# Kernel tuning notes

Hardware: AMD Instinct MI355X
Metric: run time of the kernel (lower is better)

Reference implementation:

```python
import jax, jax.numpy as jnp
import numpy as np

N = 100000      # num nodes
E = 1600000     # num edges (avg degree 16)
IN = 128        # in_channels
OUT = 64        # out_channels
HID = 2 * OUT   # conv1 output width = 2*out_channels


def setup_inputs() -> dict:
    key = jax.random.key(0)
    k0, k1, k2, k3 = jax.random.split(key, 4)
    x = jax.random.uniform(k0, (N, IN), dtype=jnp.float32)
    edge_index = jax.random.randint(k1, (2, E), 0, N, dtype=jnp.int32)
    # GCNConv weights (glorot-style uniform), biases zero-init as in PyG
    s1 = float(np.sqrt(6.0 / (IN + HID)))
    W1 = jax.random.uniform(k2, (IN, HID), minval=-s1, maxval=s1, dtype=jnp.float32)
    b1 = jnp.zeros((HID,), dtype=jnp.float32)
    s2 = float(np.sqrt(6.0 / (HID + OUT)))
    W2 = jax.random.uniform(k3, (HID, OUT), minval=-s2, maxval=s2, dtype=jnp.float32)
    b2 = jnp.zeros((OUT,), dtype=jnp.float32)
    return {"x": x, "edge_index": edge_index, "W1": W1, "b1": b1, "W2": W2, "b2": b2}


def gcn_conv(x, W, b, src, dst, n):
    """PyG GCNConv: self-loops + symmetric deg^-1/2 normalization + scatter-add."""
    h = x @ W                                   # [n, d_out] dense transform first
    loops = jnp.arange(n, dtype=src.dtype)
    s = jnp.concatenate([src, loops])           # [E+n] sources (with self-loops)
    d = jnp.concatenate([dst, loops])           # [E+n] destinations
    deg = jax.ops.segment_sum(jnp.ones_like(s, dtype=h.dtype), d, num_segments=n)
    dinv = jnp.where(deg > 0, jax.lax.rsqrt(deg), 0.0)
    norm = dinv[s] * dinv[d]                    # [E+n]
    # gather -> scale -> scatter-add aggregation
    out = jax.ops.segment_sum(h[s] * norm[:, None], d, num_segments=n)
    return out + b


def reference(x, edge_index, W1, b1, W2, b2):
    src, dst = edge_index[0], edge_index[1]
    n = x.shape[0]
    h = jax.nn.relu(gcn_conv(x, W1, b1, src, dst, n))
    return gcn_conv(h, W2, b2, src, dst, n)
```

## Files before the change

kernel.cpp:

```cpp
#include <hip/hip_runtime.h>

#define IN_C  128
#define HID_C 128
#define OUT_C 64
#define NPB      128
#define NPB_SH   7
#define NPB_MASK 127
#define MAXB     2048
#define CAP      6144
#define B1_CHUNK 8192

typedef __attribute__((ext_vector_type(8))) short short8;
typedef __attribute__((ext_vector_type(4))) float f32x4;

__device__ __forceinline__ unsigned short f2bf(float f) {
    unsigned u = __float_as_uint(f);
    unsigned r = (u + 0x7FFFu + ((u >> 16) & 1u)) >> 16;
    return (unsigned short)r;
}
__device__ __forceinline__ float bf_lo(unsigned u) { return __uint_as_float(u << 16); }
__device__ __forceinline__ float bf_hi(unsigned u) { return __uint_as_float(u & 0xFFFF0000u); }


__global__ __launch_bounds__(256) void hist_kernel(const int* __restrict__ dst,
                                                   int* __restrict__ bhist,
                                                   int E, int B) {
    __shared__ int lh[MAXB];
    int t = threadIdx.x;
    int e0 = blockIdx.x * B1_CHUNK;
    int nE = min(B1_CHUNK, E - e0);
    if (B <= MAXB) {
        for (int i = t; i < B; i += 256) lh[i] = 0;
        __syncthreads();
        for (int i = t; i < nE; i += 256) atomicAdd(&lh[dst[e0 + i] >> NPB_SH], 1);
        __syncthreads();
        for (int i = t; i < B; i += 256)
            if (lh[i]) atomicAdd(&bhist[i], lh[i]);
    } else {
        for (int i = t; i < nE; i += 256) atomicAdd(&bhist[dst[e0 + i] >> NPB_SH], 1);
    }
}

__global__ __launch_bounds__(1024) void scan_bucket_kernel(const int* __restrict__ bhist,
                                                           int* __restrict__ bbase,
                                                           int* __restrict__ bcur, int B) {
    __shared__ int sums[1024];
    int t = threadIdx.x;
    int chunk = (B + 1023) >> 10;
    int beg = t * chunk, end = min(beg + chunk, B);
    int s = 0;
    for (int i = beg; i < end; ++i) s += bhist[i];
    sums[t] = s;
    __syncthreads();
    for (int off = 1; off < 1024; off <<= 1) {
        int v = (t >= off) ? sums[t - off] : 0;
        __syncthreads();
        sums[t] += v;
        __syncthreads();
    }
    int run = (t == 0) ? 0 : sums[t - 1];
    for (int i = beg; i < end; ++i) {
        bbase[i] = run; bcur[i] = run;
        run += bhist[i];
    }
    if (t == 1023) bbase[B] = sums[1023];
}

__global__ __launch_bounds__(256) void bucket_kernel(const int* __restrict__ src,
                                                     const int* __restrict__ dst,
                                                     int* __restrict__ bcur,
                                                     int* __restrict__ ebuf,
                                                     int E, int B) {
    __shared__ int hist[MAXB];
    __shared__ int runb[MAXB];
    int t = threadIdx.x;
    int e0 = blockIdx.x * B1_CHUNK;
    int nE = min(B1_CHUNK, E - e0);
    if (B <= MAXB) {
        for (int i = t; i < B; i += 256) hist[i] = 0;
        __syncthreads();
        for (int i = t; i < nE; i += 256) atomicAdd(&hist[dst[e0 + i] >> NPB_SH], 1);
        __syncthreads();
        for (int i = t; i < B; i += 256) {
            int c = hist[i];
            runb[i] = c ? atomicAdd(&bcur[i], c) : 0;
            hist[i] = 0;
        }
        __syncthreads();
        for (int i = t; i < nE; i += 256) {
            int d = dst[e0 + i], s = src[e0 + i];
            int b = d >> NPB_SH;
            int off2 = atomicAdd(&hist[b], 1);
            ebuf[runb[b] + off2] = (s << NPB_SH) | (d & NPB_MASK);
        }
    } else {
        for (int i = t; i < nE; i += 256) {
            int d = dst[e0 + i], s = src[e0 + i];
            int pos = atomicAdd(&bcur[d >> NPB_SH], 1);
            ebuf[pos] = (s << NPB_SH) | (d & NPB_MASK);
        }
    }
}

__global__ __launch_bounds__(256) void csr_kernel(const int* __restrict__ ebuf,
                                                  const int* __restrict__ bbase,
                                                  int* __restrict__ col,
                                                  int* __restrict__ rowptr,
                                                  float* __restrict__ dinv,
                                                  int N, int E) {
    __shared__ int sorted[CAP];
    __shared__ int lhist[NPB];
    __shared__ int lpre[NPB + 1];
    int b = blockIdx.x;
    int t = threadIdx.x;
    int base = bbase[b], size = bbase[b + 1] - base;
    int node_base = b << NPB_SH;
    int nn = min(NPB, N - node_base);

    if (t < NPB) lhist[t] = 0;
    __syncthreads();
    for (int i = t; i < size; i += 256) atomicAdd(&lhist[ebuf[base + i] & NPB_MASK], 1);
    __syncthreads();
    if (t < NPB) lpre[t + 1] = lhist[t];
    if (t == 0) lpre[0] = 0;
    __syncthreads();
    for (int off = 1; off < NPB; off <<= 1) {
        int v = (t >= off && t < NPB) ? lpre[t + 1 - off] : 0;
        __syncthreads();
        if (t < NPB) lpre[t + 1] += v;
        __syncthreads();
    }
    if (t < nn) {
        rowptr[node_base + t] = base + lpre[t];
        dinv[node_base + t] = rsqrtf((float)(lhist[t] + 1));
    }
    if (node_base + nn == N && t == 0) rowptr[N] = base + size;
    if (t < NPB) lhist[t] = lpre[t];
    __syncthreads();
    if (size <= CAP) {
        for (int i = t; i < size; i += 256) {
            int entry = ebuf[base + i];
            int slot = atomicAdd(&lhist[entry & NPB_MASK], 1);
            sorted[slot] = entry >> NPB_SH;
        }
        __syncthreads();
        for (int i = t; i < size; i += 256) col[base + i] = sorted[i];
    } else {
        for (int i = t; i < size; i += 256) {
            int entry = ebuf[base + i];
            int slot = atomicAdd(&lhist[entry & NPB_MASK], 1);
            col[base + slot] = entry >> NPB_SH;
        }
    }
}


template<int C, typename InT>
__global__ __launch_bounds__(256) void mm_mfma_kernel(
    const InT* __restrict__ X, const float* __restrict__ W,
    const float* __restrict__ dinv, unsigned short* __restrict__ Hs, int n) {
    constexpr int LD = 136;
    __shared__ unsigned short Wt[C][LD];
    int t = threadIdx.x;

    for (int i = t; i < (128 * C) / 4; i += 256) {
        int idx = i * 4;
        int k = idx / C, c = idx % C;
        float4 wv = *(const float4*)&W[(size_t)k * C + c];
        Wt[c + 0][k] = f2bf(wv.x);
        Wt[c + 1][k] = f2bf(wv.y);
        Wt[c + 2][k] = f2bf(wv.z);
        Wt[c + 3][k] = f2bf(wv.w);
    }
    __syncthreads();

    int w = t >> 6, lane = t & 63;
    int m = lane & 15, quad = lane >> 4;
    int row0 = blockIdx.x * 64 + w * 16;
    int arow = min(row0 + m, n - 1);

    constexpr int NT = C / 16;
    f32x4 acc[NT];
#pragma unroll
    for (int ct = 0; ct < NT; ++ct) acc[ct] = (f32x4){0.f, 0.f, 0.f, 0.f};

#pragma unroll
    for (int kk = 0; kk < 4; ++kk) {
        int k0 = kk * 32 + quad * 8;
        short8 a;
        if constexpr (sizeof(InT) == 4) {
            const float* xp = (const float*)X + (size_t)arow * 128 + k0;
            float4 f0 = *(const float4*)xp;
            float4 f1 = *(const float4*)(xp + 4);
            a[0] = (short)f2bf(f0.x); a[1] = (short)f2bf(f0.y);
            a[2] = (short)f2bf(f0.z); a[3] = (short)f2bf(f0.w);
            a[4] = (short)f2bf(f1.x); a[5] = (short)f2bf(f1.y);
            a[6] = (short)f2bf(f1.z); a[7] = (short)f2bf(f1.w);
        } else {
            a = *(const short8*)((const unsigned short*)X + (size_t)arow * 128 + k0);
        }
#pragma unroll
        for (int ct = 0; ct < NT; ++ct) {
            short8 b = *(const short8*)&Wt[ct * 16 + m][k0];
            acc[ct] = __builtin_amdgcn_mfma_f32_16x16x32_bf16(a, b, acc[ct], 0, 0, 0);
        }
    }

    int qrow = row0 + quad * 4;
    float dv[4];
#pragma unroll
    for (int r = 0; r < 4; ++r) dv[r] = (qrow + r < n) ? dinv[qrow + r] : 0.f;
#pragma unroll
    for (int ct = 0; ct < NT; ++ct) {
        int c = ct * 16 + m;
#pragma unroll
        for (int r = 0; r < 4; ++r) {
            int row = qrow + r;
            if (row < n) Hs[(size_t)row * C + c] = f2bf(acc[ct][r] * dv[r]);
        }
    }
}


template<int C, bool BOUT>
__global__ __launch_bounds__(256) void agg_kernel(
    const unsigned short* __restrict__ Hs, const float* __restrict__ bias,
    const float* __restrict__ dinv, const int* __restrict__ rowptr,
    const int* __restrict__ col, void* __restrict__ outv, int n, int relu) {
    constexpr int LPR = C / 8;
    constexpr int SLOTS = 64 / LPR;
    int d = (blockIdx.x * 256 + threadIdx.x) >> 6;
    if (d >= n) return;
    int lane = threadIdx.x & 63;
    int cl = lane & (LPR - 1);
    int slot = lane / LPR;

    float acc[8] = {0.f, 0.f, 0.f, 0.f, 0.f, 0.f, 0.f, 0.f};
    int beg = rowptr[d], end = rowptr[d + 1];

    for (int j0 = beg; j0 < end; j0 += 64) {
        int cnt = min(64, end - j0);
        int colv = (j0 + lane < end) ? col[j0 + lane] : 0;
        int groups = (cnt + SLOTS - 1) / SLOTS;
        for (int g = 0; g < groups; g += 4) {
            uint4 v[4];
#pragma unroll
            for (int b = 0; b < 4; ++b) {
                int e = (g + b) * SLOTS + slot;
                int idx = __shfl(colv, e & 63, 64);
                bool ok = (g + b < groups) && (e < cnt);
                v[b] = ok ? *((const uint4*)(Hs + (size_t)idx * C) + cl)
                          : make_uint4(0, 0, 0, 0);
            }
#pragma unroll
            for (int b = 0; b < 4; ++b) {
                acc[0] += bf_lo(v[b].x); acc[1] += bf_hi(v[b].x);
                acc[2] += bf_lo(v[b].y); acc[3] += bf_hi(v[b].y);
                acc[4] += bf_lo(v[b].z); acc[5] += bf_hi(v[b].z);
                acc[6] += bf_lo(v[b].w); acc[7] += bf_hi(v[b].w);
            }
        }
    }
#pragma unroll
    for (int mk = LPR; mk < 64; mk <<= 1) {
#pragma unroll
        for (int k = 0; k < 8; ++k) acc[k] += __shfl_xor(acc[k], mk, 64);
    }
    uint4 sv = *((const uint4*)(Hs + (size_t)d * C) + cl);
    acc[0] += bf_lo(sv.x); acc[1] += bf_hi(sv.x);
    acc[2] += bf_lo(sv.y); acc[3] += bf_hi(sv.y);
    acc[4] += bf_lo(sv.z); acc[5] += bf_hi(sv.z);
    acc[6] += bf_lo(sv.w); acc[7] += bf_hi(sv.w);

    float dv = dinv[d];
    float4 b0 = *((const float4*)bias + cl * 2);
    float4 b1 = *((const float4*)bias + cl * 2 + 1);
    float r[8];
    r[0] = dv * acc[0] + b0.x; r[1] = dv * acc[1] + b0.y;
    r[2] = dv * acc[2] + b0.z; r[3] = dv * acc[3] + b0.w;
    r[4] = dv * acc[4] + b1.x; r[5] = dv * acc[5] + b1.y;
    r[6] = dv * acc[6] + b1.z; r[7] = dv * acc[7] + b1.w;
    if (relu) {
#pragma unroll
        for (int k = 0; k < 8; ++k) r[k] = fmaxf(r[k], 0.f);
    }
    if (slot == 0) {
        if constexpr (BOUT) {
            uint4 o;
            o.x = (unsigned)f2bf(r[0]) | ((unsigned)f2bf(r[1]) << 16);
            o.y = (unsigned)f2bf(r[2]) | ((unsigned)f2bf(r[3]) << 16);
            o.z = (unsigned)f2bf(r[4]) | ((unsigned)f2bf(r[5]) << 16);
            o.w = (unsigned)f2bf(r[6]) | ((unsigned)f2bf(r[7]) << 16);
            *(uint4*)((unsigned short*)outv + (size_t)d * C + cl * 8) = o;
        } else {
            float* o = (float*)outv + (size_t)d * C + cl * 8;
            *(float4*)o = make_float4(r[0], r[1], r[2], r[3]);
            *(float4*)(o + 4) = make_float4(r[4], r[5], r[6], r[7]);
        }
    }
}


extern "C" void kernel_launch(void* const* d_in, const int* in_sizes, int n_in,
                              void* d_out, int out_size, void* d_ws, size_t ws_size,
                              hipStream_t stream) {
    const float* x  = (const float*)d_in[0];
    const int*   ei = (const int*)d_in[1];
    const float* W1 = (const float*)d_in[2];
    const float* b1 = (const float*)d_in[3];
    const float* W2 = (const float*)d_in[4];
    const float* b2 = (const float*)d_in[5];
    float* out = (float*)d_out;

    int N = in_sizes[0] / IN_C;
    int E = in_sizes[1] / 2;
    const int* src = ei;
    const int* dst = ei + E;
    int B = (N + NPB - 1) >> NPB_SH;

    char* ws = (char*)d_ws;
    size_t off = 0;
    int*   bhist  = (int*)(ws + off);   off += (size_t)B * 4;
    int*   bbase  = (int*)(ws + off);   off += (size_t)(B + 1) * 4;
    int*   bcur   = (int*)(ws + off);   off += (size_t)B * 4;
    float* dinv   = (float*)(ws + off); off += (size_t)N * 4;
    int*   rowptr = (int*)(ws + off);   off += (size_t)(N + 1) * 4;
    off = (off + 15) & ~(size_t)15;
    int*   ebuf   = (int*)(ws + off);   off += (size_t)E * 4;
    int*   col    = (int*)(ws + off);   off += (size_t)E * 4;
    off = (off + 15) & ~(size_t)15;
    unsigned short* H1  = (unsigned short*)(ws + off); off += (size_t)N * HID_C * 2;
    off = (off + 15) & ~(size_t)15;
    unsigned short* AG1 = (unsigned short*)(ws + off); off += (size_t)N * HID_C * 2;
    unsigned short* H2 = H1;

    hipMemsetAsync(bhist, 0, (size_t)B * 4, stream);

    int nblk = (E + B1_CHUNK - 1) / B1_CHUNK;
    hist_kernel<<<nblk, 256, 0, stream>>>(dst, bhist, E, B);
    scan_bucket_kernel<<<1, 1024, 0, stream>>>(bhist, bbase, bcur, B);
    bucket_kernel<<<nblk, 256, 0, stream>>>(src, dst, bcur, ebuf, E, B);
    csr_kernel<<<B, 256, 0, stream>>>(ebuf, bbase, col, rowptr, dinv, N, E);

    int mblk = (N + 63) / 64;
    mm_mfma_kernel<HID_C, float><<<mblk, 256, 0, stream>>>(x, W1, dinv, H1, N);
    agg_kernel<HID_C, true><<<(N + 3) / 4, 256, 0, stream>>>(H1, b1, dinv, rowptr, col, AG1, N, 1);

    mm_mfma_kernel<OUT_C, unsigned short><<<mblk, 256, 0, stream>>>(AG1, W2, dinv, H2, N);
    agg_kernel<OUT_C, false><<<(N + 3) / 4, 256, 0, stream>>>(H2, b2, dinv, rowptr, col, out, N, 0);
}
```

Measured before the change: 328.3 us.

## Store hidden features in 16-column slices and aggregate per slice

Intermediate bf16 feature matrices are stored as column slices of 16 features ([slice][node][16]), and the aggregation kernel is rewritten so each block handles one slice for 128 nodes, with two threads per node walking the neighbour list serially. The aim is to keep each slice's working set (about 3.2 MB for 100k nodes) resident in cache during the random gathers. The cost is that the neighbour list is re-read once per slice, and load balance across threads now follows per-node degree instead of a wave-cooperative layout. Nontemporal loads and stores are also used for the CSR and output streams.

New measurement: 419.8 us. +27.9%, slower.

```diff
diff --git a/kernel.cpp b/kernel.cpp
--- a/kernel.cpp
+++ b/kernel.cpp
@@ -12,6 +12,7 @@
 
 typedef __attribute__((ext_vector_type(8))) short short8;
 typedef __attribute__((ext_vector_type(4))) float f32x4;
+typedef __attribute__((ext_vector_type(4))) unsigned int u32x4;
 
 __device__ __forceinline__ unsigned short f2bf(float f) {
     unsigned u = __float_as_uint(f);
@@ -197,7 +198,9 @@
             a[4] = (short)f2bf(f1.x); a[5] = (short)f2bf(f1.y);
             a[6] = (short)f2bf(f1.z); a[7] = (short)f2bf(f1.w);
         } else {
-            a = *(const short8*)((const unsigned short*)X + (size_t)arow * 128 + k0);
+            const unsigned short* xp = (const unsigned short*)X;
+            int slice = k0 >> 4;
+            a = *(const short8*)(xp + (size_t)slice * n * 16 + (size_t)arow * 16 + (k0 & 15));
         }
 #pragma unroll
         for (int ct = 0; ct < NT; ++ct) {
@@ -212,69 +215,71 @@
     for (int r = 0; r < 4; ++r) dv[r] = (qrow + r < n) ? dinv[qrow + r] : 0.f;
 #pragma unroll
     for (int ct = 0; ct < NT; ++ct) {
-        int c = ct * 16 + m;
+        unsigned short* hp = Hs + (size_t)ct * n * 16 + m;
 #pragma unroll
         for (int r = 0; r < 4; ++r) {
             int row = qrow + r;
-            if (row < n) Hs[(size_t)row * C + c] = f2bf(acc[ct][r] * dv[r]);
+            if (row < n) hp[(size_t)row * 16] = f2bf(acc[ct][r] * dv[r]);
         }
     }
 }
 
 
 template<int C, bool BOUT>
-__global__ __launch_bounds__(256) void agg_kernel(
+__global__ __launch_bounds__(256) void agg_slice_kernel(
     const unsigned short* __restrict__ Hs, const float* __restrict__ bias,
     const float* __restrict__ dinv, const int* __restrict__ rowptr,
     const int* __restrict__ col, void* __restrict__ outv, int n, int relu) {
-    constexpr int LPR = C / 8;
-    constexpr int SLOTS = 64 / LPR;
-    int d = (blockIdx.x * 256 + threadIdx.x) >> 6;
+    constexpr int NS = C / 16;
+    int sb = blockIdx.x % NS;
+    int blk = blockIdx.x / NS;
+    int d = blk * 128 + (threadIdx.x >> 1);
     if (d >= n) return;
-    int lane = threadIdx.x & 63;
-    int cl = lane & (LPR - 1);
-    int slot = lane / LPR;
-
-    float acc[8] = {0.f, 0.f, 0.f, 0.f, 0.f, 0.f, 0.f, 0.f};
-    int beg = rowptr[d], end = rowptr[d + 1];
-
-    for (int j0 = beg; j0 < end; j0 += 64) {
-        int cnt = min(64, end - j0);
-        int colv = (j0 + lane < end) ? col[j0 + lane] : 0;
-        int groups = (cnt + SLOTS - 1) / SLOTS;
-        for (int g = 0; g < groups; g += 4) {
-            uint4 v[4];
-#pragma unroll
-            for (int b = 0; b < 4; ++b) {
-                int e = (g + b) * SLOTS + slot;
-                int idx = __shfl(colv, e & 63, 64);
-                bool ok = (g + b < groups) && (e < cnt);
-                v[b] = ok ? *((const uint4*)(Hs + (size_t)idx * C) + cl)
-                          : make_uint4(0, 0, 0, 0);
-            }
-#pragma unroll
-            for (int b = 0; b < 4; ++b) {
-                acc[0] += bf_lo(v[b].x); acc[1] += bf_hi(v[b].x);
-                acc[2] += bf_lo(v[b].y); acc[3] += bf_hi(v[b].y);
-                acc[4] += bf_lo(v[b].z); acc[5] += bf_hi(v[b].z);
-                acc[6] += bf_lo(v[b].w); acc[7] += bf_hi(v[b].w);
-            }
-        }
-    }
-#pragma unroll
-    for (int mk = LPR; mk < 64; mk <<= 1) {
-#pragma unroll
-        for (int k = 0; k < 8; ++k) acc[k] += __shfl_xor(acc[k], mk, 64);
-    }
-    uint4 sv = *((const uint4*)(Hs + (size_t)d * C) + cl);
-    acc[0] += bf_lo(sv.x); acc[1] += bf_hi(sv.x);
-    acc[2] += bf_lo(sv.y); acc[3] += bf_hi(sv.y);
-    acc[4] += bf_lo(sv.z); acc[5] += bf_hi(sv.z);
-    acc[6] += bf_lo(sv.w); acc[7] += bf_hi(sv.w);
+    int half = threadIdx.x & 1;
+    const unsigned short* hsl = Hs + (size_t)sb * n * 16;
+
+    int beg = __builtin_nontemporal_load(&rowptr[d]);
+    int end = __builtin_nontemporal_load(&rowptr[d + 1]);
+
+    float acc[8];
+    uint4 v0 = *((const uint4*)(hsl + (size_t)d * 16) + half);
+    acc[0] = bf_lo(v0.x); acc[1] = bf_hi(v0.x);
+    acc[2] = bf_lo(v0.y); acc[3] = bf_hi(v0.y);
+    acc[4] = bf_lo(v0.z); acc[5] = bf_hi(v0.z);
+    acc[6] = bf_lo(v0.w); acc[7] = bf_hi(v0.w);
+
+    int j = beg;
+    for (; j + 4 <= end; j += 4) {
+        int c0 = __builtin_nontemporal_load(col + j);
+        int c1 = __builtin_nontemporal_load(col + j + 1);
+        int c2 = __builtin_nontemporal_load(col + j + 2);
+        int c3 = __builtin_nontemporal_load(col + j + 3);
+        uint4 v[4];
+        v[0] = *((const uint4*)(hsl + (size_t)c0 * 16) + half);
+        v[1] = *((const uint4*)(hsl + (size_t)c1 * 16) + half);
+        v[2] = *((const uint4*)(hsl + (size_t)c2 * 16) + half);
+        v[3] = *((const uint4*)(hsl + (size_t)c3 * 16) + half);
+#pragma unroll
+        for (int b = 0; b < 4; ++b) {
+            acc[0] += bf_lo(v[b].x); acc[1] += bf_hi(v[b].x);
+            acc[2] += bf_lo(v[b].y); acc[3] += bf_hi(v[b].y);
+            acc[4] += bf_lo(v[b].z); acc[5] += bf_hi(v[b].z);
+            acc[6] += bf_lo(v[b].w); acc[7] += bf_hi(v[b].w);
+        }
+    }
+    for (; j < end; ++j) {
+        int c0 = __builtin_nontemporal_load(col + j);
+        uint4 v = *((const uint4*)(hsl + (size_t)c0 * 16) + half);
+        acc[0] += bf_lo(v.x); acc[1] += bf_hi(v.x);
+        acc[2] += bf_lo(v.y); acc[3] += bf_hi(v.y);
+        acc[4] += bf_lo(v.z); acc[5] += bf_hi(v.z);
+        acc[6] += bf_lo(v.w); acc[7] += bf_hi(v.w);
+    }
 
     float dv = dinv[d];
-    float4 b0 = *((const float4*)bias + cl * 2);
-    float4 b1 = *((const float4*)bias + cl * 2 + 1);
+    const float* bp = bias + sb * 16 + half * 8;
+    float4 b0 = *(const float4*)bp;
+    float4 b1 = *(const float4*)(bp + 4);
     float r[8];
     r[0] = dv * acc[0] + b0.x; r[1] = dv * acc[1] + b0.y;
     r[2] = dv * acc[2] + b0.z; r[3] = dv * acc[3] + b0.w;
@@ -284,19 +289,20 @@
 #pragma unroll
         for (int k = 0; k < 8; ++k) r[k] = fmaxf(r[k], 0.f);
     }
-    if (slot == 0) {
-        if constexpr (BOUT) {
-            uint4 o;
-            o.x = (unsigned)f2bf(r[0]) | ((unsigned)f2bf(r[1]) << 16);
-            o.y = (unsigned)f2bf(r[2]) | ((unsigned)f2bf(r[3]) << 16);
-            o.z = (unsigned)f2bf(r[4]) | ((unsigned)f2bf(r[5]) << 16);
-            o.w = (unsigned)f2bf(r[6]) | ((unsigned)f2bf(r[7]) << 16);
-            *(uint4*)((unsigned short*)outv + (size_t)d * C + cl * 8) = o;
-        } else {
-            float* o = (float*)outv + (size_t)d * C + cl * 8;
-            *(float4*)o = make_float4(r[0], r[1], r[2], r[3]);
-            *(float4*)(o + 4) = make_float4(r[4], r[5], r[6], r[7]);
-        }
+    if constexpr (BOUT) {
+        u32x4 o;
+        o.x = (unsigned)f2bf(r[0]) | ((unsigned)f2bf(r[1]) << 16);
+        o.y = (unsigned)f2bf(r[2]) | ((unsigned)f2bf(r[3]) << 16);
+        o.z = (unsigned)f2bf(r[4]) | ((unsigned)f2bf(r[5]) << 16);
+        o.w = (unsigned)f2bf(r[6]) | ((unsigned)f2bf(r[7]) << 16);
+        u32x4* op = (u32x4*)((unsigned short*)outv + (size_t)sb * n * 16 + (size_t)d * 16 + half * 8);
+        __builtin_nontemporal_store(o, op);
+    } else {
+        float* o = (float*)outv + (size_t)d * C + sb * 16 + half * 8;
+        f32x4 o0 = {r[0], r[1], r[2], r[3]};
+        f32x4 o1 = {r[4], r[5], r[6], r[7]};
+        __builtin_nontemporal_store(o0, (f32x4*)o);
+        __builtin_nontemporal_store(o1, (f32x4*)o + 1);
     }
 }
 
@@ -343,9 +349,13 @@
     csr_kernel<<<B, 256, 0, stream>>>(ebuf, bbase, col, rowptr, dinv, N, E);
 
     int mblk = (N + 63) / 64;
+    int ablk = (N + 127) >> 7;
+
     mm_mfma_kernel<HID_C, float><<<mblk, 256, 0, stream>>>(x, W1, dinv, H1, N);
-    agg_kernel<HID_C, true><<<(N + 3) / 4, 256, 0, stream>>>(H1, b1, dinv, rowptr, col, AG1, N, 1);
+    agg_slice_kernel<HID_C, true><<<ablk * (HID_C / 16), 256, 0, stream>>>(
+        H1, b1, dinv, rowptr, col, AG1, N, 1);
 
     mm_mfma_kernel<OUT_C, unsigned short><<<mblk, 256, 0, stream>>>(AG1, W2, dinv, H2, N);
-    agg_kernel<OUT_C, false><<<(N + 3) / 4, 256, 0, stream>>>(H2, b2, dinv, rowptr, col, out, N, 0);
-}
+    agg_slice_kernel<OUT_C, false><<<ablk * (OUT_C / 16), 256, 0, stream>>>(
+        H2, b2, dinv, rowptr, col, out, N, 0);
+}
```

## Pad CSR rows to multiples of 16 with zero-row sentinel to remove gather predication

Applied to the files above, without the earlier changes.

Each node's neighbour list is padded up to a multiple of 16 entries, and the padding points at an extra all-zero row appended to H. This lets the aggregation loop drop per-edge bounds checks and run full unrolled gather groups. The separate ebuf is removed so bucketing and CSR sorting work in place in col. The bucket chunk and shared-memory sort capacity are also retuned. The trade-off is extra padded gathers of the zero row and a larger col array. The in-place fallback path for oversized buckets only handles up to 32 entries per thread.

Result: slower. 347.3 us (+5.8%).

```diff
diff --git a/kernel.cpp b/kernel.cpp
--- a/kernel.cpp
+++ b/kernel.cpp
@@ -7,8 +7,10 @@
 #define NPB_SH   7
 #define NPB_MASK 127
 #define MAXB     2048
-#define CAP      6144
-#define B1_CHUNK 8192
+#define CAP      8192
+#define B1_CHUNK 4096
+#define PADQ     16
+#define PADSLACK ((PADQ - 1) * NPB)
 
 typedef __attribute__((ext_vector_type(8))) short short8;
 typedef __attribute__((ext_vector_type(4))) float f32x4;
@@ -60,7 +62,8 @@
     }
     int run = (t == 0) ? 0 : sums[t - 1];
     for (int i = beg; i < end; ++i) {
-        bbase[i] = run; bcur[i] = run;
+        bbase[i] = run;
+        bcur[i] = run + i * PADSLACK;
         run += bhist[i];
     }
     if (t == 1023) bbase[B] = sums[1023];
@@ -69,7 +72,7 @@
 __global__ __launch_bounds__(256) void bucket_kernel(const int* __restrict__ src,
                                                      const int* __restrict__ dst,
                                                      int* __restrict__ bcur,
-                                                     int* __restrict__ ebuf,
+                                                     int* __restrict__ col,
                                                      int E, int B) {
     __shared__ int hist[MAXB];
     __shared__ int runb[MAXB];
@@ -91,21 +94,21 @@
             int d = dst[e0 + i], s = src[e0 + i];
             int b = d >> NPB_SH;
             int off2 = atomicAdd(&hist[b], 1);
-            ebuf[runb[b] + off2] = (s << NPB_SH) | (d & NPB_MASK);
+            col[runb[b] + off2] = (s << NPB_SH) | (d & NPB_MASK);
         }
     } else {
         for (int i = t; i < nE; i += 256) {
             int d = dst[e0 + i], s = src[e0 + i];
             int pos = atomicAdd(&bcur[d >> NPB_SH], 1);
-            ebuf[pos] = (s << NPB_SH) | (d & NPB_MASK);
-        }
-    }
-}
-
-__global__ __launch_bounds__(256) void csr_kernel(const int* __restrict__ ebuf,
+            col[pos] = (s << NPB_SH) | (d & NPB_MASK);
+        }
+    }
+}
+
+__global__ __launch_bounds__(256) void csr_kernel(int* __restrict__ col,
                                                   const int* __restrict__ bbase,
-                                                  int* __restrict__ col,
                                                   int* __restrict__ rowptr,
+                                                  int* __restrict__ rowend,
                                                   float* __restrict__ dinv,
                                                   int N, int E) {
     __shared__ int sorted[CAP];
@@ -113,15 +116,16 @@
     __shared__ int lpre[NPB + 1];
     int b = blockIdx.x;
     int t = threadIdx.x;
-    int base = bbase[b], size = bbase[b + 1] - base;
+    int size = bbase[b + 1] - bbase[b];
+    int pbase = bbase[b] + b * PADSLACK;
     int node_base = b << NPB_SH;
     int nn = min(NPB, N - node_base);
 
     if (t < NPB) lhist[t] = 0;
     __syncthreads();
-    for (int i = t; i < size; i += 256) atomicAdd(&lhist[ebuf[base + i] & NPB_MASK], 1);
-    __syncthreads();
-    if (t < NPB) lpre[t + 1] = lhist[t];
+    for (int i = t; i < size; i += 256) atomicAdd(&lhist[col[pbase + i] & NPB_MASK], 1);
+    __syncthreads();
+    if (t < NPB) lpre[t + 1] = (lhist[t] + PADQ - 1) & ~(PADQ - 1);
     if (t == 0) lpre[0] = 0;
     __syncthreads();
     for (int off = 1; off < NPB; off <<= 1) {
@@ -131,25 +135,35 @@
         __syncthreads();
     }
     if (t < nn) {
-        rowptr[node_base + t] = base + lpre[t];
+        rowptr[node_base + t] = pbase + lpre[t];
+        rowend[node_base + t] = pbase + lpre[t + 1];
         dinv[node_base + t] = rsqrtf((float)(lhist[t] + 1));
     }
-    if (node_base + nn == N && t == 0) rowptr[N] = base + size;
     if (t < NPB) lhist[t] = lpre[t];
     __syncthreads();
-    if (size <= CAP) {
+    int psize = lpre[NPB];
+    if (psize <= CAP) {
+        for (int i = t; i < psize; i += 256) sorted[i] = N;
+        __syncthreads();
         for (int i = t; i < size; i += 256) {
-            int entry = ebuf[base + i];
+            int entry = col[pbase + i];
             int slot = atomicAdd(&lhist[entry & NPB_MASK], 1);
             sorted[slot] = entry >> NPB_SH;
         }
         __syncthreads();
-        for (int i = t; i < size; i += 256) col[base + i] = sorted[i];
+        for (int i = t; i < psize; i += 256) col[pbase + i] = sorted[i];
     } else {
-        for (int i = t; i < size; i += 256) {
-            int entry = ebuf[base + i];
+        int ent[32];
+        int c2 = 0;
+        for (int i = t; i < size && c2 < 32; i += 256) ent[c2++] = col[pbase + i];
+        __syncthreads();
+        for (int i = t; i < psize; i += 256) col[pbase + i] = N;
+        __syncthreads();
+        c2 = 0;
+        for (int i = t; i < size && c2 < 32; i += 256) {
+            int entry = ent[c2++];
             int slot = atomicAdd(&lhist[entry & NPB_MASK], 1);
-            col[base + slot] = entry >> NPB_SH;
+            col[pbase + slot] = entry >> NPB_SH;
         }
     }
 }
@@ -162,6 +176,11 @@
     constexpr int LD = 136;
     __shared__ unsigned short Wt[C][LD];
     int t = threadIdx.x;
+
+    if (blockIdx.x == 0) {
+        for (int i = t; i < C / 2; i += 256)
+            ((unsigned*)(Hs + (size_t)n * C))[i] = 0;
+    }
 
     for (int i = t; i < (128 * C) / 4; i += 256) {
         int idx = i * 4;
@@ -222,11 +241,28 @@
 }
 
 
+#define GBODY(NB)                                                              \
+    {                                                                          \
+        uint4 v[NB];                                                           \
+        _Pragma("unroll") for (int b = 0; b < NB; ++b) {                       \
+            int e = (g + b) * SLOTS + slot;                                    \
+            int idx = __shfl(colv, e, 64);                                     \
+            v[b] = *((const uint4*)(Hs + (size_t)idx * C) + cl);               \
+        }                                                                      \
+        _Pragma("unroll") for (int b = 0; b < NB; ++b) {                       \
+            acc[0] += bf_lo(v[b].x); acc[1] += bf_hi(v[b].x);                  \
+            acc[2] += bf_lo(v[b].y); acc[3] += bf_hi(v[b].y);                  \
+            acc[4] += bf_lo(v[b].z); acc[5] += bf_hi(v[b].z);                  \
+            acc[6] += bf_lo(v[b].w); acc[7] += bf_hi(v[b].w);                  \
+        }                                                                      \
+    }
+
 template<int C, bool BOUT>
 __global__ __launch_bounds__(256) void agg_kernel(
     const unsigned short* __restrict__ Hs, const float* __restrict__ bias,
     const float* __restrict__ dinv, const int* __restrict__ rowptr,
-    const int* __restrict__ col, void* __restrict__ outv, int n, int relu) {
+    const int* __restrict__ rowend, const int* __restrict__ col,
+    void* __restrict__ outv, int n, int relu) {
     constexpr int LPR = C / 8;
     constexpr int SLOTS = 64 / LPR;
     int d = (blockIdx.x * 256 + threadIdx.x) >> 6;
@@ -236,29 +272,16 @@
     int slot = lane / LPR;
 
     float acc[8] = {0.f, 0.f, 0.f, 0.f, 0.f, 0.f, 0.f, 0.f};
-    int beg = rowptr[d], end = rowptr[d + 1];
+    int beg = rowptr[d], end = rowend[d];
 
     for (int j0 = beg; j0 < end; j0 += 64) {
         int cnt = min(64, end - j0);
-        int colv = (j0 + lane < end) ? col[j0 + lane] : 0;
-        int groups = (cnt + SLOTS - 1) / SLOTS;
-        for (int g = 0; g < groups; g += 4) {
-            uint4 v[4];
-#pragma unroll
-            for (int b = 0; b < 4; ++b) {
-                int e = (g + b) * SLOTS + slot;
-                int idx = __shfl(colv, e & 63, 64);
-                bool ok = (g + b < groups) && (e < cnt);
-                v[b] = ok ? *((const uint4*)(Hs + (size_t)idx * C) + cl)
-                          : make_uint4(0, 0, 0, 0);
-            }
-#pragma unroll
-            for (int b = 0; b < 4; ++b) {
-                acc[0] += bf_lo(v[b].x); acc[1] += bf_hi(v[b].x);
-                acc[2] += bf_lo(v[b].y); acc[3] += bf_hi(v[b].y);
-                acc[4] += bf_lo(v[b].z); acc[5] += bf_hi(v[b].z);
-                acc[6] += bf_lo(v[b].w); acc[7] += bf_hi(v[b].w);
-            }
+        int colv = col[j0 + lane];
+        int groups = cnt / SLOTS;
+        int g = 0;
+        for (; g + 4 <= groups; g += 4) GBODY(4)
+        if constexpr (SLOTS == 8) {
+            if (g < groups) GBODY(2)
         }
     }
 #pragma unroll
@@ -317,6 +340,7 @@
     const int* src = ei;
     const int* dst = ei + E;
     int B = (N + NPB - 1) >> NPB_SH;
+    int nblk = (E + B1_CHUNK - 1) / B1_CHUNK;
 
     char* ws = (char*)d_ws;
     size_t off = 0;
@@ -324,28 +348,29 @@
     int*   bbase  = (int*)(ws + off);   off += (size_t)(B + 1) * 4;
     int*   bcur   = (int*)(ws + off);   off += (size_t)B * 4;
     float* dinv   = (float*)(ws + off); off += (size_t)N * 4;
-    int*   rowptr = (int*)(ws + off);   off += (size_t)(N + 1) * 4;
+    int*   rowptr = (int*)(ws + off);   off += (size_t)N * 4;
+    int*   rowend = (int*)(ws + off);   off += (size_t)N * 4;
     off = (off + 15) & ~(size_t)15;
-    int*   ebuf   = (int*)(ws + off);   off += (size_t)E * 4;
-    int*   col    = (int*)(ws + off);   off += (size_t)E * 4;
+    int*   col    = (int*)(ws + off);   off += ((size_t)E + (size_t)B * PADSLACK + 64) * 4;
     off = (off + 15) & ~(size_t)15;
-    unsigned short* H1  = (unsigned short*)(ws + off); off += (size_t)N * HID_C * 2;
+    unsigned short* H1  = (unsigned short*)(ws + off); off += (size_t)(N + 1) * HID_C * 2;
     off = (off + 15) & ~(size_t)15;
     unsigned short* AG1 = (unsigned short*)(ws + off); off += (size_t)N * HID_C * 2;
     unsigned short* H2 = H1;
 
     hipMemsetAsync(bhist, 0, (size_t)B * 4, stream);
 
-    int nblk = (E + B1_CHUNK - 1) / B1_CHUNK;
     hist_kernel<<<nblk, 256, 0, stream>>>(dst, bhist, E, B);
     scan_bucket_kernel<<<1, 1024, 0, stream>>>(bhist, bbase, bcur, B);
-    bucket_kernel<<<nblk, 256, 0, stream>>>(src, dst, bcur, ebuf, E, B);
-    csr_kernel<<<B, 256, 0, stream>>>(ebuf, bbase, col, rowptr, dinv, N, E);
+    bucket_kernel<<<nblk, 256, 0, stream>>>(src, dst, bcur, col, E, B);
+    csr_kernel<<<B, 256, 0, stream>>>(col, bbase, rowptr, rowend, dinv, N, E);
 
     int mblk = (N + 63) / 64;
     mm_mfma_kernel<HID_C, float><<<mblk, 256, 0, stream>>>(x, W1, dinv, H1, N);
-    agg_kernel<HID_C, true><<<(N + 3) / 4, 256, 0, stream>>>(H1, b1, dinv, rowptr, col, AG1, N, 1);
+    agg_kernel<HID_C, true><<<(N + 3) / 4, 256, 0, stream>>>(
+        H1, b1, dinv, rowptr, rowend, col, AG1, N, 1);
 
     mm_mfma_kernel<OUT_C, unsigned short><<<mblk, 256, 0, stream>>>(AG1, W2, dinv, H2, N);
-    agg_kernel<OUT_C, false><<<(N + 3) / 4, 256, 0, stream>>>(H2, b2, dinv, rowptr, col, out, N, 0);
-}
+    agg_kernel<OUT_C, false><<<(N + 3) / 4, 256, 0, stream>>>(
+        H2, b2, dinv, rowptr, rowend, col, out, N, 0);
+}
```
